# Kernel tuning notes

Measured on AMD Instinct MI355X. Metric: run time of the kernel, lower is better.

## Reference

```python
import jax, jax.numpy as jnp
import numpy as np

HIDDEN = 512
TEMPERATURE = float(np.sqrt(HIDDEN))  # scaled-dot temperature
BATCH = 64


def _build_weights(attn_weight, N, K):
    """Vectorized version of get_attn_weight: (S,S,H) with S = N*K+1.
    Regions: 0=same_sample, 1=same_class, 2=diff_class, 3=support->query,
    4=query->support, 5=query->query. Replicates the torch overwrite order."""
    S = N * K + 1
    NK = N * K
    i = jnp.arange(S)[:, None]
    j = jnp.arange(S)[None, :]
    idx = jnp.full((S, S), 2, dtype=jnp.int32)                      # w_diff_class
    idx = jnp.where((i // K) == (j // K), 1, idx)                   # w_same_class
    idx = jnp.where((i < NK) & (j == NK), 3, idx)                   # w_stoquery
    idx = jnp.where(i == j, 0, idx)                                 # w_same_sample (diag)
    idx = jnp.where((i == NK) & (j < NK), 4, idx)                   # w_querytos
    idx = jnp.where((i == NK) & (j == NK), 5, idx)                  # w_query
    return attn_weight[idx]  # (S, S, H)


def setup_inputs() -> dict:
    key = jax.random.key(0)
    kq, kk, kv, kw = jax.random.split(key, 4)
    N, K = 10, 10
    S = N * K + 1  # 101
    q = jax.random.normal(kq, (BATCH, S, HIDDEN), dtype=jnp.float32)
    k = jax.random.normal(kk, (BATCH, S, HIDDEN), dtype=jnp.float32)
    v = jax.random.normal(kv, (BATCH, S, HIDDEN), dtype=jnp.float32)
    bound = float(np.sqrt(6 / 2))
    attn_weight = jax.random.uniform(kw, (6, HIDDEN), dtype=jnp.float32,
                                     minval=-bound, maxval=bound)
    return {"q": q, "k": k, "v": v, "attn_weight": attn_weight, "N": N, "K": K}


def reference(q, k, v, attn_weight, N, K):
    # attn[b,i,j] = softmax_j(q.k^T / temperature)
    scores = jnp.einsum("bih,bjh->bij", q, k) / TEMPERATURE
    attn = jax.nn.softmax(scores, axis=2)  # dropout p=0 (eval) -> identity
    weights = _build_weights(attn_weight, N, K)  # (S,S,H)
    # out[b,i,h] = sum_j attn[b,i,j] * weights[i,j,h] * v[b,j,h]
    out = jnp.einsum("bij,ijh,bjh->bih", attn, weights, v)
    return out, attn
```

## Files before the change

kernel.cpp:

```cpp
#include <hip/hip_runtime.h>
#include <math.h>
#include <stdint.h>

#define BATCH 64
#define SEQ   101
#define HID   512
#define NKQ   100
#define KCLS  10
#define INV_TEMP 0.04419417382415922f

typedef short bf16x8 __attribute__((ext_vector_type(8)));
typedef float f32x4  __attribute__((ext_vector_type(4)));

__device__ inline void split_bf16(float x, short& hi, short& lo) {
    uint32_t u = __builtin_bit_cast(uint32_t, x);
    hi = (short)(u >> 16);
    float hf = __builtin_bit_cast(float, u & 0xFFFF0000u);
    float l  = x - hf;
    lo = (short)(__builtin_bit_cast(uint32_t, l) >> 16);
}
__device__ inline short rtn_bf16(float x) {
    uint32_t u = __builtin_bit_cast(uint32_t, x);
    return (short)((u + 0x7FFFu + ((u >> 16) & 1u)) >> 16);
}

#define KCH 64
#define KST 72
#define VST 72
#define VRS 132

#define OFF_QHI 18432
#define OFF_QLO 20736
#define OFF_VTH 33792
#define OFF_VTL 52224
#define POOLSZ  70656

__global__ __launch_bounds__(512, 4)
void fused_attn(const float* __restrict__ q, const float* __restrict__ k,
                const float* __restrict__ v, const float* __restrict__ aw,
                float* __restrict__ out, float* __restrict__ attn) {
    __shared__ __align__(16) char pool[POOLSZ];
    __shared__ __align__(16) float sc[16][132];
    short (*khi)[KST]  = (short(*)[KST])(pool);
    short (*qhi)[KST]  = (short(*)[KST])(pool + OFF_QHI);
    short (*qlo)[KST]  = (short(*)[KST])(pool + OFF_QLO);
    float (*vraw)[VRS] = (float(*)[VRS])(pool);
    short (*vth)[VST]  = (short(*)[VST])(pool + OFF_VTH);
    short (*vtl)[VST]  = (short(*)[VST])(pool + OFF_VTL);

    const int b   = blockIdx.x & 63;
    const int i0  = (blockIdx.x >> 6) * 16;
    const int tid = threadIdx.x;
    const int wv  = tid >> 6, lane = tid & 63;
    const int m   = lane & 15;
    const int kq  = (lane >> 4) * 8;
    const int rq  = (lane >> 4) * 4;
    const int j0w = wv * 16;

    const float* qb = q + (size_t)b * SEQ * HID;
    const float* kb = k + (size_t)b * SEQ * HID;
    const float* vb = v + (size_t)b * SEQ * HID;

    f32x4 acc = {};
    for (int kc = 0; kc < HID; kc += KCH) {
        #pragma unroll
        for (int s = 0; s < 4; ++s) {
            const int f = tid + s * 512;
            const int r = f >> 4, c = (f & 15) << 2;
            float4 x = make_float4(0.f, 0.f, 0.f, 0.f);
            if (r < SEQ) x = *(const float4*)(kb + (size_t)r * HID + kc + c);
            short4 hv;
            hv.x = rtn_bf16(x.x); hv.y = rtn_bf16(x.y);
            hv.z = rtn_bf16(x.z); hv.w = rtn_bf16(x.w);
            *(short4*)&khi[r][c] = hv;
        }
        if (tid < 256) {
            const int r = tid >> 4, c = (tid & 15) << 2;
            const int gi = i0 + r;
            float4 x = make_float4(0.f, 0.f, 0.f, 0.f);
            if (gi < SEQ) x = *(const float4*)(qb + (size_t)gi * HID + kc + c);
            short4 hv, lv;
            split_bf16(x.x, hv.x, lv.x);
            split_bf16(x.y, hv.y, lv.y);
            split_bf16(x.z, hv.z, lv.z);
            split_bf16(x.w, hv.w, lv.w);
            *(short4*)&qhi[r][c] = hv;
            *(short4*)&qlo[r][c] = lv;
        }
        __syncthreads();
        #pragma unroll
        for (int ks = 0; ks < KCH; ks += 32) {
            const bf16x8 qH = *(const bf16x8*)&qhi[m][ks + kq];
            const bf16x8 qL = *(const bf16x8*)&qlo[m][ks + kq];
            const bf16x8 kH = *(const bf16x8*)&khi[j0w + m][ks + kq];
            acc = __builtin_amdgcn_mfma_f32_16x16x32_bf16(qH, kH, acc, 0, 0, 0);
            acc = __builtin_amdgcn_mfma_f32_16x16x32_bf16(qL, kH, acc, 0, 0, 0);
        }
        __syncthreads();
    }
    #pragma unroll
    for (int r = 0; r < 4; ++r)
        sc[rq + r][j0w + m] = acc[r];
    __syncthreads();

    {
        const int row = tid >> 5, t32 = tid & 31;
        const int gi  = i0 + row;
        float mx = -1e30f;
        for (int j = t32; j < SEQ; j += 32) {
            float s = sc[row][j] * INV_TEMP;
            sc[row][j] = s;
            mx = fmaxf(mx, s);
        }
        #pragma unroll
        for (int off = 1; off < 32; off <<= 1) mx = fmaxf(mx, __shfl_xor(mx, off));
        float sum = 0.f;
        for (int j = t32; j < SEQ; j += 32) {
            float e = __expf(sc[row][j] - mx);
            sc[row][j] = e;
            sum += e;
        }
        #pragma unroll
        for (int off = 1; off < 32; off <<= 1) sum += __shfl_xor(sum, off);
        const float inv = 1.f / sum;
        float* arow = attn + ((size_t)b * SEQ + gi) * SEQ;
        for (int j = t32; j < SEQ; j += 32) {
            float a = sc[row][j] * inv;
            sc[row][j] = a;
            if (gi < SEQ) arow[j] = a;
        }
        for (int j = SEQ + t32; j < 128; j += 32) sc[row][j] = 0.f;
    }
    __syncthreads();

    int ai = i0 + m; if (ai > NKQ) ai = NKQ;
    const int ci = ai / KCLS;
    uint32_t mbits = 0;
    #pragma unroll
    for (int ks = 0; ks < 4; ++ks)
        #pragma unroll
        for (int e = 0; e < 8; ++e)
            if (((ks * 32 + kq + e) / KCLS) == ci) mbits |= (1u << (ks * 8 + e));
    bf16x8 Ah[4], Al[4];
    #pragma unroll
    for (int ks = 0; ks < 4; ++ks) {
        const f32x4 u0 = *(const f32x4*)&sc[m][ks * 32 + kq];
        const f32x4 u1 = *(const f32x4*)&sc[m][ks * 32 + kq + 4];
        const float x[8] = {u0[0], u0[1], u0[2], u0[3], u1[0], u1[1], u1[2], u1[3]};
        #pragma unroll
        for (int e = 0; e < 8; ++e) {
            short h, l; split_bf16(x[e], h, l);
            Ah[ks][e] = h; Al[ks][e] = l;
        }
    }

    for (int hc = 0; hc < 4; ++hc) {
        const int hbase = hc << 7;
        f32x4 T = {}, U = {};
        #pragma unroll
        for (int half = 0; half < 2; ++half) {
            __syncthreads();
            #pragma unroll
            for (int s = 0; s < 4; ++s) {
                const int f = tid + s * 512;
                const int j = f >> 5, h4 = (f & 31) << 2;
                const int jg = half * 64 + j;
                float4 x = make_float4(0.f, 0.f, 0.f, 0.f);
                if (jg < SEQ) x = *(const float4*)(vb + (size_t)jg * HID + hbase + h4);
                *(float4*)&vraw[j][h4] = x;
            }
            __syncthreads();
            #pragma unroll
            for (int s = 0; s < 4; ++s) {
                const int it = tid + s * 512;
                const int h = it & 127, jl = (it >> 7) << 2;
                short4 hv, lv;
                split_bf16(vraw[jl + 0][h], hv.x, lv.x);
                split_bf16(vraw[jl + 1][h], hv.y, lv.y);
                split_bf16(vraw[jl + 2][h], hv.z, lv.z);
                split_bf16(vraw[jl + 3][h], hv.w, lv.w);
                *(short4*)&vth[h][jl] = hv;
                *(short4*)&vtl[h][jl] = lv;
            }
            __syncthreads();
            #pragma unroll
            for (int ksl = 0; ksl < 2; ++ksl) {
                const int ks = half * 2 + ksl;
                const bf16x8 Bh = *(const bf16x8*)&vth[j0w + m][ksl * 32 + kq];
                const bf16x8 Bl = *(const bf16x8*)&vtl[j0w + m][ksl * 32 + kq];
                bf16x8 Mh;
                #pragma unroll
                for (int e = 0; e < 8; ++e)
                    Mh[e] = (mbits & (1u << (ks * 8 + e))) ? Ah[ks][e] : (short)0;
                T = __builtin_amdgcn_mfma_f32_16x16x32_bf16(Ah[ks], Bh, T, 0, 0, 0);
                T = __builtin_amdgcn_mfma_f32_16x16x32_bf16(Ah[ks], Bl, T, 0, 0, 0);
                T = __builtin_amdgcn_mfma_f32_16x16x32_bf16(Al[ks], Bh, T, 0, 0, 0);
                U = __builtin_amdgcn_mfma_f32_16x16x32_bf16(Mh,     Bh, U, 0, 0, 0);
            }
        }
        const int h = hbase + j0w + m;
        const float w0 = aw[0 * HID + h], w1 = aw[1 * HID + h], w2 = aw[2 * HID + h];
        const float w3 = aw[3 * HID + h], w4 = aw[4 * HID + h], w5 = aw[5 * HID + h];
        const float vN = vb[(size_t)NKQ * HID + h];
        #pragma unroll
        for (int r = 0; r < 4; ++r) {
            const int i = i0 + rq + r;
            if (i >= SEQ) continue;
            const int il = rq + r;
            const float t = T[r], u = U[r];
            const float aiN = sc[il][NKQ];
            float o;
            if (i < NKQ) {
                const float aii = sc[il][i];
                const float vi  = vb[(size_t)i * HID + h];
                o = w2 * t + (w1 - w2) * u + (w0 - w1) * aii * vi + (w3 - w2) * aiN * vN;
            } else {
                o = w4 * t + (w5 - w4) * aiN * vN;
            }
            out[((size_t)b * SEQ + i) * HID + h] = o;
        }
    }
}

extern "C" void kernel_launch(void* const* d_in, const int* in_sizes, int n_in,
                              void* d_out, int out_size, void* d_ws, size_t ws_size,
                              hipStream_t stream) {
    const float* q  = (const float*)d_in[0];
    const float* k  = (const float*)d_in[1];
    const float* v  = (const float*)d_in[2];
    const float* aw = (const float*)d_in[3];
    float* out  = (float*)d_out;
    float* attn = out + (size_t)BATCH * SEQ * HID;
    (void)d_ws; (void)ws_size;

    fused_attn<<<dim3(448), dim3(512), 0, stream>>>(q, k, v, aw, out, attn);
}
```

Before: 122.8 us.

## Load K directly into MFMA registers, stage Q once, prefetch V with swizzled LDS

The QK^T phase now keeps the whole 16-row Q tile split into hi/lo bf16 in LDS. Each wave reads its K rows straight from global memory into registers with a one-step software prefetch and packs them using v_cvt_pk_bf16_f32. This removes the per-chunk K staging and its barriers. The PV phase is flattened into eight steps that prefetch the next V tile into registers while the current one is computed. V is written raw into a swizzled LDS layout and split into hi/lo per lane, which drops the separate transposed vth/vtl buffers and one barrier per step. K rounding now uses the hardware conversion instead of manual round-to-nearest-even, and the direct global K loads may be less coalesced than before.

```diff
diff --git a/kernel.cpp b/kernel.cpp
--- a/kernel.cpp
+++ b/kernel.cpp
@@ -11,7 +11,13 @@
 
 typedef short bf16x8 __attribute__((ext_vector_type(8)));
 typedef float f32x4  __attribute__((ext_vector_type(4)));
-
+typedef uint32_t u32x4 __attribute__((ext_vector_type(4)));
+
+__device__ inline uint32_t cvt2(float a, float b) {
+    uint32_t r;
+    asm("v_cvt_pk_bf16_f32 %0, %1, %2" : "=v"(r) : "v"(a), "v"(b));
+    return r;
+}
 __device__ inline void split_bf16(float x, short& hi, short& lo) {
     uint32_t u = __builtin_bit_cast(uint32_t, x);
     hi = (short)(u >> 16);
@@ -19,21 +25,26 @@
     float l  = x - hf;
     lo = (short)(__builtin_bit_cast(uint32_t, l) >> 16);
 }
-__device__ inline short rtn_bf16(float x) {
-    uint32_t u = __builtin_bit_cast(uint32_t, x);
-    return (short)((u + 0x7FFFu + ((u >> 16) & 1u)) >> 16);
-}
-
-#define KCH 64
-#define KST 72
-#define VST 72
+
+#define QST 520
 #define VRS 132
 
-#define OFF_QHI 18432
-#define OFF_QLO 20736
-#define OFF_VTH 33792
-#define OFF_VTL 52224
-#define POOLSZ  70656
+#define OFF_QLO 16640
+#define POOLSZ  33792
+
+__device__ inline void vload(const float* __restrict__ vb, int tid, int step,
+                             f32x4 pf[4]) {
+    const int half = step & 1, hb = (step >> 1) << 7;
+    #pragma unroll
+    for (int s = 0; s < 4; ++s) {
+        const int f = tid + s * 512;
+        const int j = f >> 5, h4 = (f & 31) << 2;
+        const int jg = half * 64 + j;
+        f32x4 x = {};
+        if (jg < SEQ) x = *(const f32x4*)(vb + (size_t)jg * HID + hb + h4);
+        pf[s] = x;
+    }
+}
 
 __global__ __launch_bounds__(512, 4)
 void fused_attn(const float* __restrict__ q, const float* __restrict__ k,
@@ -41,62 +52,65 @@
                 float* __restrict__ out, float* __restrict__ attn) {
     __shared__ __align__(16) char pool[POOLSZ];
     __shared__ __align__(16) float sc[16][132];
-    short (*khi)[KST]  = (short(*)[KST])(pool);
-    short (*qhi)[KST]  = (short(*)[KST])(pool + OFF_QHI);
-    short (*qlo)[KST]  = (short(*)[KST])(pool + OFF_QLO);
+    short (*qhi)[QST]  = (short(*)[QST])(pool);
+    short (*qlo)[QST]  = (short(*)[QST])(pool + OFF_QLO);
     float (*vraw)[VRS] = (float(*)[VRS])(pool);
-    short (*vth)[VST]  = (short(*)[VST])(pool + OFF_VTH);
-    short (*vtl)[VST]  = (short(*)[VST])(pool + OFF_VTL);
 
     const int b   = blockIdx.x & 63;
     const int i0  = (blockIdx.x >> 6) * 16;
     const int tid = threadIdx.x;
     const int wv  = tid >> 6, lane = tid & 63;
     const int m   = lane & 15;
-    const int kq  = (lane >> 4) * 8;
-    const int rq  = (lane >> 4) * 4;
+    const int g   = lane >> 4;
+    const int kq  = g * 8;
+    const int rq  = g * 4;
     const int j0w = wv * 16;
 
     const float* qb = q + (size_t)b * SEQ * HID;
     const float* kb = k + (size_t)b * SEQ * HID;
     const float* vb = v + (size_t)b * SEQ * HID;
 
+    #pragma unroll
+    for (int s = 0; s < 4; ++s) {
+        const int f = tid + s * 512;
+        const int r = f >> 7, c = (f & 127) << 2;
+        const int gi = i0 + r;
+        f32x4 x = {};
+        if (gi < SEQ) x = *(const f32x4*)(qb + (size_t)gi * HID + c);
+        short4 hv, lv;
+        split_bf16(x[0], hv.x, lv.x);
+        split_bf16(x[1], hv.y, lv.y);
+        split_bf16(x[2], hv.z, lv.z);
+        split_bf16(x[3], hv.w, lv.w);
+        *(short4*)&qhi[r][c] = hv;
+        *(short4*)&qlo[r][c] = lv;
+    }
+    __syncthreads();
+
     f32x4 acc = {};
-    for (int kc = 0; kc < HID; kc += KCH) {
-        #pragma unroll
-        for (int s = 0; s < 4; ++s) {
-            const int f = tid + s * 512;
-            const int r = f >> 4, c = (f & 15) << 2;
-            float4 x = make_float4(0.f, 0.f, 0.f, 0.f);
-            if (r < SEQ) x = *(const float4*)(kb + (size_t)r * HID + kc + c);
-            short4 hv;
-            hv.x = rtn_bf16(x.x); hv.y = rtn_bf16(x.y);
-            hv.z = rtn_bf16(x.z); hv.w = rtn_bf16(x.w);
-            *(short4*)&khi[r][c] = hv;
-        }
-        if (tid < 256) {
-            const int r = tid >> 4, c = (tid & 15) << 2;
-            const int gi = i0 + r;
-            float4 x = make_float4(0.f, 0.f, 0.f, 0.f);
-            if (gi < SEQ) x = *(const float4*)(qb + (size_t)gi * HID + kc + c);
-            short4 hv, lv;
-            split_bf16(x.x, hv.x, lv.x);
-            split_bf16(x.y, hv.y, lv.y);
-            split_bf16(x.z, hv.z, lv.z);
-            split_bf16(x.w, hv.w, lv.w);
-            *(short4*)&qhi[r][c] = hv;
-            *(short4*)&qlo[r][c] = lv;
-        }
-        __syncthreads();
-        #pragma unroll
-        for (int ks = 0; ks < KCH; ks += 32) {
-            const bf16x8 qH = *(const bf16x8*)&qhi[m][ks + kq];
-            const bf16x8 qL = *(const bf16x8*)&qlo[m][ks + kq];
-            const bf16x8 kH = *(const bf16x8*)&khi[j0w + m][ks + kq];
+    {
+        const int jg = j0w + m;
+        const int jr = (jg > NKQ) ? NKQ : jg;
+        const float* kr = kb + (size_t)jr * HID + kq;
+        f32x4 k0 = *(const f32x4*)(kr);
+        f32x4 k1 = *(const f32x4*)(kr + 4);
+        #pragma unroll
+        for (int ks = 0; ks < 16; ++ks) {
+            f32x4 n0 = {}, n1 = {};
+            if (ks < 15) {
+                n0 = *(const f32x4*)(kr + (ks + 1) * 32);
+                n1 = *(const f32x4*)(kr + (ks + 1) * 32 + 4);
+            }
+            u32x4 kp;
+            kp[0] = cvt2(k0[0], k0[1]); kp[1] = cvt2(k0[2], k0[3]);
+            kp[2] = cvt2(k1[0], k1[1]); kp[3] = cvt2(k1[2], k1[3]);
+            const bf16x8 kH = __builtin_bit_cast(bf16x8, kp);
+            const bf16x8 qH = *(const bf16x8*)&qhi[m][ks * 32 + kq];
+            const bf16x8 qL = *(const bf16x8*)&qlo[m][ks * 32 + kq];
             acc = __builtin_amdgcn_mfma_f32_16x16x32_bf16(qH, kH, acc, 0, 0, 0);
             acc = __builtin_amdgcn_mfma_f32_16x16x32_bf16(qL, kH, acc, 0, 0, 0);
-        }
-        __syncthreads();
+            k0 = n0; k1 = n1;
+        }
     }
     #pragma unroll
     for (int r = 0; r < 4; ++r)
@@ -154,70 +168,74 @@
         }
     }
 
-    for (int hc = 0; hc < 4; ++hc) {
-        const int hbase = hc << 7;
-        f32x4 T = {}, U = {};
-        #pragma unroll
-        for (int half = 0; half < 2; ++half) {
-            __syncthreads();
+    const int hl   = j0w + m;
+    const int rcol = (hl + 8 * g) & 127;
+    f32x4 pf[4];
+    vload(vb, tid, 0, pf);
+    f32x4 T = {}, U = {};
+    for (int step = 0; step < 8; ++step) {
+        const int half = step & 1, hc = step >> 1;
+        __syncthreads();
+        #pragma unroll
+        for (int s = 0; s < 4; ++s) {
+            const int f = tid + s * 512;
+            const int j = f >> 5, h4 = (f & 31) << 2;
+            const int col = (h4 + 8 * ((j >> 3) & 3)) & 127;
+            *(f32x4*)&vraw[j][col] = pf[s];
+        }
+        __syncthreads();
+        if (step < 7) vload(vb, tid, step + 1, pf);
+
+        #pragma unroll
+        for (int ksl = 0; ksl < 2; ++ksl) {
+            const int ks = half * 2 + ksl;
+            const int jb = ksl * 32 + kq;
+            u32x4 ph, pl;
             #pragma unroll
-            for (int s = 0; s < 4; ++s) {
-                const int f = tid + s * 512;
-                const int j = f >> 5, h4 = (f & 31) << 2;
-                const int jg = half * 64 + j;
-                float4 x = make_float4(0.f, 0.f, 0.f, 0.f);
-                if (jg < SEQ) x = *(const float4*)(vb + (size_t)jg * HID + hbase + h4);
-                *(float4*)&vraw[j][h4] = x;
+            for (int p = 0; p < 4; ++p) {
+                const float x0 = vraw[jb + 2 * p][rcol];
+                const float x1 = vraw[jb + 2 * p + 1][rcol];
+                const uint32_t h01 = cvt2(x0, x1);
+                const float r0 = x0 - __builtin_bit_cast(float, h01 << 16);
+                const float r1 = x1 - __builtin_bit_cast(float, h01 & 0xFFFF0000u);
+                ph[p] = h01;
+                pl[p] = cvt2(r0, r1);
             }
-            __syncthreads();
+            const bf16x8 Bh = __builtin_bit_cast(bf16x8, ph);
+            const bf16x8 Bl = __builtin_bit_cast(bf16x8, pl);
+            bf16x8 Mh;
             #pragma unroll
-            for (int s = 0; s < 4; ++s) {
-                const int it = tid + s * 512;
-                const int h = it & 127, jl = (it >> 7) << 2;
-                short4 hv, lv;
-                split_bf16(vraw[jl + 0][h], hv.x, lv.x);
-                split_bf16(vraw[jl + 1][h], hv.y, lv.y);
-                split_bf16(vraw[jl + 2][h], hv.z, lv.z);
-                split_bf16(vraw[jl + 3][h], hv.w, lv.w);
-                *(short4*)&vth[h][jl] = hv;
-                *(short4*)&vtl[h][jl] = lv;
+            for (int e = 0; e < 8; ++e)
+                Mh[e] = (mbits & (1u << (ks * 8 + e))) ? Ah[ks][e] : (short)0;
+            T = __builtin_amdgcn_mfma_f32_16x16x32_bf16(Ah[ks], Bh, T, 0, 0, 0);
+            T = __builtin_amdgcn_mfma_f32_16x16x32_bf16(Ah[ks], Bl, T, 0, 0, 0);
+            T = __builtin_amdgcn_mfma_f32_16x16x32_bf16(Al[ks], Bh, T, 0, 0, 0);
+            U = __builtin_amdgcn_mfma_f32_16x16x32_bf16(Mh,     Bh, U, 0, 0, 0);
+        }
+
+        if (half == 1) {
+            const int h = (hc << 7) + hl;
+            const float w0 = aw[0 * HID + h], w1 = aw[1 * HID + h], w2 = aw[2 * HID + h];
+            const float w3 = aw[3 * HID + h], w4 = aw[4 * HID + h], w5 = aw[5 * HID + h];
+            const float vN = vb[(size_t)NKQ * HID + h];
+            #pragma unroll
+            for (int r = 0; r < 4; ++r) {
+                const int i = i0 + rq + r;
+                if (i >= SEQ) continue;
+                const int il = rq + r;
+                const float t = T[r], u = U[r];
+                const float aiN = sc[il][NKQ];
+                float o;
+                if (i < NKQ) {
+                    const float aii = sc[il][i];
+                    const float vi  = vb[(size_t)i * HID + h];
+                    o = w2 * t + (w1 - w2) * u + (w0 - w1) * aii * vi + (w3 - w2) * aiN * vN;
+                } else {
+                    o = w4 * t + (w5 - w4) * aiN * vN;
+                }
+                out[((size_t)b * SEQ + i) * HID + h] = o;
             }
-            __syncthreads();
-            #pragma unroll
-            for (int ksl = 0; ksl < 2; ++ksl) {
-                const int ks = half * 2 + ksl;
-                const bf16x8 Bh = *(const bf16x8*)&vth[j0w + m][ksl * 32 + kq];
-                const bf16x8 Bl = *(const bf16x8*)&vtl[j0w + m][ksl * 32 + kq];
-                bf16x8 Mh;
-                #pragma unroll
-                for (int e = 0; e < 8; ++e)
-                    Mh[e] = (mbits & (1u << (ks * 8 + e))) ? Ah[ks][e] : (short)0;
-                T = __builtin_amdgcn_mfma_f32_16x16x32_bf16(Ah[ks], Bh, T, 0, 0, 0);
-                T = __builtin_amdgcn_mfma_f32_16x16x32_bf16(Ah[ks], Bl, T, 0, 0, 0);
-                T = __builtin_amdgcn_mfma_f32_16x16x32_bf16(Al[ks], Bh, T, 0, 0, 0);
-                U = __builtin_amdgcn_mfma_f32_16x16x32_bf16(Mh,     Bh, U, 0, 0, 0);
-            }
-        }
-        const int h = hbase + j0w + m;
-        const float w0 = aw[0 * HID + h], w1 = aw[1 * HID + h], w2 = aw[2 * HID + h];
-        const float w3 = aw[3 * HID + h], w4 = aw[4 * HID + h], w5 = aw[5 * HID + h];
-        const float vN = vb[(size_t)NKQ * HID + h];
-        #pragma unroll
-        for (int r = 0; r < 4; ++r) {
-            const int i = i0 + rq + r;
-            if (i >= SEQ) continue;
-            const int il = rq + r;
-            const float t = T[r], u = U[r];
-            const float aiN = sc[il][NKQ];
-            float o;
-            if (i < NKQ) {
-                const float aii = sc[il][i];
-                const float vi  = vb[(size_t)i * HID + h];
-                o = w2 * t + (w1 - w2) * u + (w0 - w1) * aii * vi + (w3 - w2) * aiN * vN;
-            } else {
-                o = w4 * t + (w5 - w4) * aiN * vN;
-            }
-            out[((size_t)b * SEQ + i) * HID + h] = o;
+            T = (f32x4){}; U = (f32x4){};
         }
     }
 }
```

Measured after the change: 266.0 us. +116.6%, slower.
